# Kernel optimization log

Measured on AMD Instinct MI355X. Metric: run time of the kernel, lower is better.

The kernel has to match this reference:

```python
import jax, jax.numpy as jnp
import numpy as np

NB, S, D, B, T, KMAX = 7, 16, 128, 32, 2048, 31
KS = [31, 21, 15, 11, 7, 5, 3]  # per-band conv kernel sizes


def _ln(x, g, b, eps=1e-5):
    m = x.mean(-1, keepdims=True)
    v = ((x - m) ** 2).mean(-1, keepdims=True)
    return (x - m) * jax.lax.rsqrt(v + eps) * g + b


def setup_inputs() -> dict:
    key = jax.random.key(0)
    ks = jax.random.split(key, 18)
    n = lambda k, shape, s=0.02: jax.random.normal(k, shape, jnp.float32) * s
    # conv kernels zero-padded to KMAX=31; symmetric padding keeps SAME-conv
    # equivalent to Conv1d(kernel=k, padding=k//2)
    mask = np.zeros((NB, KMAX, 1, 1), np.float32)
    for i, k in enumerate(KS):
        off = (KMAX - k) // 2
        mask[i, off:off + k] = 1.0
    inp = {
        'x': jax.random.normal(ks[0], (B, T, S), jnp.float32),
        'conv_w': n(ks[1], (NB, KMAX, S, D)) * jnp.asarray(mask),
        'conv_b': n(ks[2], (NB, D)),
        'dec_g': jnp.ones((NB, D), jnp.float32),
        'dec_b': jnp.zeros((NB, D), jnp.float32),
        'n2_g': jnp.ones((NB, D), jnp.float32),
        'n2_b': jnp.zeros((NB, D), jnp.float32),
        'ffn_w1': n(ks[3], (NB, D, 2 * D)),
        'ffn_b1': n(ks[4], (NB, 2 * D)),
        'ffn_w2': n(ks[5], (NB, 2 * D, D)),
        'ffn_b2': n(ks[6], (NB, D)),
        'proj_w': n(ks[7], (NB, D, 4 * S)),
        'proj_b': n(ks[8], (NB, 4 * S)),
        'mix_w1': n(ks[9], (NB * 4 * S, 8 * S)),
        'mix_b1': n(ks[10], (8 * S,)),
        'mix_w2': n(ks[11], (8 * S, S)),
        'mix_b2': n(ks[12], (S,)),
    }
    return inp


def reference(x, conv_w, conv_b, dec_g, dec_b, n2_g, n2_b,
              ffn_w1, ffn_b1, ffn_w2, ffn_b2,
              proj_w, proj_b, mix_w1, mix_b1, mix_w2, mix_b2):
    # Spectral decomposition: per-band 1D conv + LayerNorm. [nb, B, T, D]
    conv1 = lambda w: jax.lax.conv_general_dilated(
        x, w, (1,), 'SAME', dimension_numbers=('NWC', 'WIO', 'NWC'))
    h = jax.vmap(conv1)(conv_w) + conv_b[:, None, None, :]
    h = _ln(h, dec_g[:, None, None, :], dec_b[:, None, None, :])
    # Band processors (empty history => residual FFN branch)
    z = _ln(h, n2_g[:, None, None, :], n2_b[:, None, None, :])
    u = jax.nn.gelu(jnp.einsum('nbtd,nde->nbte', z, ffn_w1)
                    + ffn_b1[:, None, None, :], approximate=False)
    band_out = h + (jnp.einsum('nbte,ned->nbtd', u, ffn_w2)
                    + ffn_b2[:, None, None, :])
    # Reconstruction: per-band projection, concat, mix MLP
    p = jnp.einsum('nbtd,ndp->nbtp', band_out, proj_w) + proj_b[:, None, None, :]
    cat = jnp.transpose(p, (1, 2, 0, 3)).reshape(x.shape[0], x.shape[1], -1)
    m = jax.nn.gelu(cat @ mix_w1 + mix_b1, approximate=False)
    return m @ mix_w2 + mix_b2
```

## Files before the change

kernel.cpp:

```cpp
#include <hip/hip_runtime.h>
#include <stdint.h>

#define NB   7
#define SIN  16
#define DD   128
#define BB   32
#define TT   2048
#define TM   64
#define KMAX 31

#define XWS  40
#define HS   136
#define US   264
#define PS   72

#define O_CWT 0
#define O_W1T 458752
#define O_W2T 688128
#define O_PT  917504
#define O_M1T 974848
#define O_M2T 1032192
#define W_TOTAL 1034240

typedef short v8s __attribute__((ext_vector_type(8)));
typedef float v4f __attribute__((ext_vector_type(4)));

__device__ __forceinline__ unsigned short f2b(float f) {
    unsigned u = __float_as_uint(f);
    u += 0x7fffu + ((u >> 16) & 1u);
    return (unsigned short)(u >> 16);
}
__device__ __forceinline__ float b2f(unsigned short h) {
    return __uint_as_float(((unsigned)h) << 16);
}
__device__ __forceinline__ float gelu_fast(float x) {
    return x / (1.f + __expf(-1.702f * x));
}
__device__ __forceinline__ float gelu_exact(float x) {
    return 0.5f * x * (1.f + erff(x * 0.70710678118654752f));
}

__global__ void prep_weights(const float* __restrict__ conv_w,
                             const float* __restrict__ ffn_w1,
                             const float* __restrict__ ffn_w2,
                             const float* __restrict__ proj_w,
                             const float* __restrict__ mix_w1,
                             const float* __restrict__ mix_w2,
                             unsigned short* __restrict__ wsb) {
    for (int i = blockIdx.x * 256 + threadIdx.x; i < W_TOTAL; i += gridDim.x * 256) {
        float v;
        int o = i;
        if (o < O_W1T) {
            int n = o / (128 * 512); int r = o % (128 * 512);
            int d = r / 512; int kf = r % 512;
            int k = kf >> 4, s = kf & 15;
            v = (k < KMAX) ? conv_w[((n * KMAX + k) * SIN + s) * DD + d] : 0.f;
        } else if ((o -= O_W1T) < (O_W2T - O_W1T)) {
            int n = o / (256 * 128); int r = o % (256 * 128);
            int e = r / 128; int k = r % 128;
            v = ffn_w1[(n * 128 + k) * 256 + e];
        } else if ((o -= (O_W2T - O_W1T)) < (O_PT - O_W2T)) {
            int n = o / (128 * 256); int r = o % (128 * 256);
            int d = r / 256; int e = r % 256;
            v = ffn_w2[(n * 256 + e) * 128 + d];
        } else if ((o -= (O_PT - O_W2T)) < (O_M1T - O_PT)) {
            int n = o / (64 * 128); int r = o % (64 * 128);
            int j = r / 128; int k = r % 128;
            v = proj_w[(n * 128 + k) * 64 + j];
        } else if ((o -= (O_M1T - O_PT)) < (O_M2T - O_M1T)) {
            int c = o / 448; int kk = o % 448;
            v = mix_w1[kk * 128 + c];
        } else {
            o -= (O_M2T - O_M1T);
            int o16 = o / 128; int c = o % 128;
            v = mix_w2[c * 16 + o16];
        }
        wsb[i] = f2b(v);
    }
}

__global__ __launch_bounds__(256, 2)
void fused_main(const float* __restrict__ x,
                const float* __restrict__ conv_b,
                const float* __restrict__ dec_g, const float* __restrict__ dec_b,
                const float* __restrict__ n2_g,  const float* __restrict__ n2_b,
                const float* __restrict__ ffn_b1, const float* __restrict__ ffn_b2,
                const float* __restrict__ proj_b,
                const float* __restrict__ mix_b1, const float* __restrict__ mix_b2,
                const unsigned short* __restrict__ wsb,
                float* __restrict__ out) {
    __shared__ __align__(16) unsigned short xw[95 * XWS];
    __shared__ __align__(16) unsigned short hbuf[TM * HS];
    __shared__ __align__(16) unsigned short zbuf[TM * HS];
    __shared__ __align__(16) unsigned short ubuf[TM * US];

    const int tid  = threadIdx.x;
    const int lane = tid & 63;
    const int w    = tid >> 6;
    const int l16  = lane & 15;
    const int quad = lane >> 4;
    const int bb   = blockIdx.x >> 5;
    const int t0   = (blockIdx.x & 31) * TM;

    const unsigned short* cwT = wsb + O_CWT;
    const unsigned short* w1T = wsb + O_W1T;
    const unsigned short* w2T = wsb + O_W2T;
    const unsigned short* pT  = wsb + O_PT;
    const unsigned short* m1T = wsb + O_M1T;
    const unsigned short* m2T = wsb + O_M2T;

    for (int i = tid; i < 95 * SIN; i += 256) {
        int r = i >> 4, s = i & 15;
        int t = t0 + r - 15;
        float v = (t >= 0 && t < TT) ? x[((long)bb * TT + t) * SIN + s] : 0.f;
        xw[r * XWS + s] = f2b(v);
    }

    v4f macc[4][2];
    #pragma unroll
    for (int a = 0; a < 4; a++)
        #pragma unroll
        for (int c = 0; c < 2; c++)
            macc[a][c] = (v4f){0.f, 0.f, 0.f, 0.f};

    __syncthreads();

    static const int lo_tab[NB] = {0, 64, 128, 160, 192, 192, 224};
    static const int hi_tab[NB] = {512, 416, 384, 352, 320, 288, 288};

    for (int n = 0; n < NB; ++n) {
        {
            v4f acc[4][2];
            #pragma unroll
            for (int mt = 0; mt < 4; mt++)
                #pragma unroll
                for (int nt = 0; nt < 2; nt++) acc[mt][nt] = (v4f){0.f, 0.f, 0.f, 0.f};
            const int colb = w * 32;
            const int lo = lo_tab[n], hi = hi_tab[n];
            for (int kf = lo; kf < hi; kf += 32) {
                const int tap  = (kf >> 4) + (quad >> 1);
                const int scol = (quad & 1) * 8;
                v8s a[4], bf[2];
                #pragma unroll
                for (int mt = 0; mt < 4; mt++)
                    a[mt] = *reinterpret_cast<const v8s*>(&xw[(mt * 16 + l16 + tap) * XWS + scol]);
                #pragma unroll
                for (int nt = 0; nt < 2; nt++)
                    bf[nt] = *reinterpret_cast<const v8s*>(
                        &cwT[(size_t)(n * 128 + colb + nt * 16 + l16) * 512 + kf + quad * 8]);
                #pragma unroll
                for (int mt = 0; mt < 4; mt++)
                    #pragma unroll
                    for (int nt = 0; nt < 2; nt++)
                        acc[mt][nt] = __builtin_amdgcn_mfma_f32_16x16x32_bf16(a[mt], bf[nt], acc[mt][nt], 0, 0, 0);
            }
            #pragma unroll
            for (int nt = 0; nt < 2; nt++) {
                const int col = colb + nt * 16 + l16;
                const float bias = conv_b[n * 128 + col];
                #pragma unroll
                for (int mt = 0; mt < 4; mt++)
                    #pragma unroll
                    for (int r = 0; r < 4; r++)
                        hbuf[(mt * 16 + quad * 4 + r) * HS + col] = f2b(acc[mt][nt][r] + bias);
            }
        }
        __syncthreads();

        {
            const int row = tid >> 2, q = tid & 3;
            float v[32], s1 = 0.f, s2 = 0.f;
            #pragma unroll
            for (int c8 = 0; c8 < 4; c8++) {
                v8s t8 = *reinterpret_cast<const v8s*>(&hbuf[row * HS + q * 32 + c8 * 8]);
                #pragma unroll
                for (int j = 0; j < 8; j++) {
                    float f = b2f((unsigned short)t8[j]);
                    v[c8 * 8 + j] = f; s1 += f; s2 += f * f;
                }
            }
            s1 += __shfl_xor(s1, 1); s2 += __shfl_xor(s2, 1);
            s1 += __shfl_xor(s1, 2); s2 += __shfl_xor(s2, 2);
            const float m1 = s1 * (1.f / 128.f);
            const float rs = rsqrtf(s2 * (1.f / 128.f) - m1 * m1 + 1e-5f);
            const float4* dg4 = (const float4*)(dec_g + n * 128);
            const float4* db4 = (const float4*)(dec_b + n * 128);
            float hv[32], t1 = 0.f, t2 = 0.f;
            #pragma unroll
            for (int c4 = 0; c4 < 8; c4++) {
                float4 g4 = dg4[q * 8 + c4], b4 = db4[q * 8 + c4];
                float ga[4] = {g4.x, g4.y, g4.z, g4.w};
                float ba[4] = {b4.x, b4.y, b4.z, b4.w};
                #pragma unroll
                for (int j = 0; j < 4; j++) {
                    float h = (v[c4 * 4 + j] - m1) * rs * ga[j] + ba[j];
                    hv[c4 * 4 + j] = h; t1 += h; t2 += h * h;
                    hbuf[row * HS + q * 32 + c4 * 4 + j] = f2b(h);
                }
            }
            t1 += __shfl_xor(t1, 1); t2 += __shfl_xor(t2, 1);
            t1 += __shfl_xor(t1, 2); t2 += __shfl_xor(t2, 2);
            const float m2 = t1 * (1.f / 128.f);
            const float rs2 = rsqrtf(t2 * (1.f / 128.f) - m2 * m2 + 1e-5f);
            const float4* ng4 = (const float4*)(n2_g + n * 128);
            const float4* nb4 = (const float4*)(n2_b + n * 128);
            #pragma unroll
            for (int c4 = 0; c4 < 8; c4++) {
                float4 g4 = ng4[q * 8 + c4], b4 = nb4[q * 8 + c4];
                float ga[4] = {g4.x, g4.y, g4.z, g4.w};
                float ba[4] = {b4.x, b4.y, b4.z, b4.w};
                #pragma unroll
                for (int j = 0; j < 4; j++) {
                    float z = (hv[c4 * 4 + j] - m2) * rs2 * ga[j] + ba[j];
                    zbuf[row * HS + q * 32 + c4 * 4 + j] = f2b(z);
                }
            }
        }
        __syncthreads();

        {
            v4f acc[4][4];
            #pragma unroll
            for (int mt = 0; mt < 4; mt++)
                #pragma unroll
                for (int et = 0; et < 4; et++) acc[mt][et] = (v4f){0.f, 0.f, 0.f, 0.f};
            const int eb = w * 64;
            #pragma unroll
            for (int kb = 0; kb < 128; kb += 32) {
                v8s a[4], bf[4];
                #pragma unroll
                for (int mt = 0; mt < 4; mt++)
                    a[mt] = *reinterpret_cast<const v8s*>(&zbuf[(mt * 16 + l16) * HS + kb + quad * 8]);
                #pragma unroll
                for (int et = 0; et < 4; et++)
                    bf[et] = *reinterpret_cast<const v8s*>(
                        &w1T[(size_t)(n * 256 + eb + et * 16 + l16) * 128 + kb + quad * 8]);
                #pragma unroll
                for (int mt = 0; mt < 4; mt++)
                    #pragma unroll
                    for (int et = 0; et < 4; et++)
                        acc[mt][et] = __builtin_amdgcn_mfma_f32_16x16x32_bf16(a[mt], bf[et], acc[mt][et], 0, 0, 0);
            }
            #pragma unroll
            for (int et = 0; et < 4; et++) {
                const int e = eb + et * 16 + l16;
                const float bias = ffn_b1[n * 256 + e];
                #pragma unroll
                for (int mt = 0; mt < 4; mt++)
                    #pragma unroll
                    for (int r = 0; r < 4; r++)
                        ubuf[(mt * 16 + quad * 4 + r) * US + e] = f2b(gelu_fast(acc[mt][et][r] + bias));
            }
        }
        __syncthreads();

        {
            v4f acc[4][2];
            #pragma unroll
            for (int mt = 0; mt < 4; mt++)
                #pragma unroll
                for (int nt = 0; nt < 2; nt++) acc[mt][nt] = (v4f){0.f, 0.f, 0.f, 0.f};
            const int dbs = w * 32;
            #pragma unroll
            for (int kb = 0; kb < 256; kb += 32) {
                v8s a[4], bf[2];
                #pragma unroll
                for (int mt = 0; mt < 4; mt++)
                    a[mt] = *reinterpret_cast<const v8s*>(&ubuf[(mt * 16 + l16) * US + kb + quad * 8]);
                #pragma unroll
                for (int nt = 0; nt < 2; nt++)
                    bf[nt] = *reinterpret_cast<const v8s*>(
                        &w2T[(size_t)(n * 128 + dbs + nt * 16 + l16) * 256 + kb + quad * 8]);
                #pragma unroll
                for (int mt = 0; mt < 4; mt++)
                    #pragma unroll
                    for (int nt = 0; nt < 2; nt++)
                        acc[mt][nt] = __builtin_amdgcn_mfma_f32_16x16x32_bf16(a[mt], bf[nt], acc[mt][nt], 0, 0, 0);
            }
            #pragma unroll
            for (int nt = 0; nt < 2; nt++) {
                const int col = dbs + nt * 16 + l16;
                const float bias = ffn_b2[n * 128 + col];
                #pragma unroll
                for (int mt = 0; mt < 4; mt++)
                    #pragma unroll
                    for (int r = 0; r < 4; r++) {
                        const int row = mt * 16 + quad * 4 + r;
                        float bo = acc[mt][nt][r] + bias + b2f(hbuf[row * HS + col]);
                        zbuf[row * HS + col] = f2b(bo);
                    }
            }
        }
        __syncthreads();

        {
            v4f acc[4];
            #pragma unroll
            for (int mt = 0; mt < 4; mt++) acc[mt] = (v4f){0.f, 0.f, 0.f, 0.f};
            const int j = w * 16 + l16;
            #pragma unroll
            for (int kb = 0; kb < 128; kb += 32) {
                v8s bf = *reinterpret_cast<const v8s*>(&pT[(size_t)(n * 64 + j) * 128 + kb + quad * 8]);
                #pragma unroll
                for (int mt = 0; mt < 4; mt++) {
                    v8s a = *reinterpret_cast<const v8s*>(&zbuf[(mt * 16 + l16) * HS + kb + quad * 8]);
                    acc[mt] = __builtin_amdgcn_mfma_f32_16x16x32_bf16(a, bf, acc[mt], 0, 0, 0);
                }
            }
            const float bias = proj_b[n * 64 + j];
            unsigned short* pb = ubuf;
            #pragma unroll
            for (int mt = 0; mt < 4; mt++)
                #pragma unroll
                for (int r = 0; r < 4; r++)
                    pb[(mt * 16 + quad * 4 + r) * PS + j] = f2b(acc[mt][r] + bias);
        }
        __syncthreads();

        {
            const unsigned short* pb = ubuf;
            #pragma unroll
            for (int kb = 0; kb < 64; kb += 32) {
                v8s a[4], bf[2];
                #pragma unroll
                for (int mt = 0; mt < 4; mt++)
                    a[mt] = *reinterpret_cast<const v8s*>(&pb[(mt * 16 + l16) * PS + kb + quad * 8]);
                #pragma unroll
                for (int nt = 0; nt < 2; nt++)
                    bf[nt] = *reinterpret_cast<const v8s*>(
                        &m1T[(size_t)(w * 32 + nt * 16 + l16) * 448 + n * 64 + kb + quad * 8]);
                #pragma unroll
                for (int mt = 0; mt < 4; mt++)
                    #pragma unroll
                    for (int nt = 0; nt < 2; nt++)
                        macc[mt][nt] = __builtin_amdgcn_mfma_f32_16x16x32_bf16(a[mt], bf[nt], macc[mt][nt], 0, 0, 0);
            }
        }
    }

    #pragma unroll
    for (int nt = 0; nt < 2; nt++) {
        const int col = w * 32 + nt * 16 + l16;
        const float bias = mix_b1[col];
        #pragma unroll
        for (int mt = 0; mt < 4; mt++)
            #pragma unroll
            for (int r = 0; r < 4; r++)
                zbuf[(mt * 16 + quad * 4 + r) * HS + col] = f2b(gelu_exact(macc[mt][nt][r] + bias));
    }
    __syncthreads();

    {
        v4f acc = (v4f){0.f, 0.f, 0.f, 0.f};
        #pragma unroll
        for (int kb = 0; kb < 128; kb += 32) {
            v8s a  = *reinterpret_cast<const v8s*>(&zbuf[(w * 16 + l16) * HS + kb + quad * 8]);
            v8s bf = *reinterpret_cast<const v8s*>(&m2T[(size_t)l16 * 128 + kb + quad * 8]);
            acc = __builtin_amdgcn_mfma_f32_16x16x32_bf16(a, bf, acc, 0, 0, 0);
        }
        const float bias = mix_b2[l16];
        #pragma unroll
        for (int r = 0; r < 4; r++) {
            const int row = w * 16 + quad * 4 + r;
            out[((long)bb * TT + t0 + row) * SIN + l16] = acc[r] + bias;
        }
    }
}

extern "C" void kernel_launch(void* const* d_in, const int* in_sizes, int n_in,
                              void* d_out, int out_size, void* d_ws, size_t ws_size,
                              hipStream_t stream) {
    (void)in_sizes; (void)n_in; (void)out_size; (void)ws_size;
    const float* x      = (const float*)d_in[0];
    const float* conv_w = (const float*)d_in[1];
    const float* conv_b = (const float*)d_in[2];
    const float* dec_g  = (const float*)d_in[3];
    const float* dec_b  = (const float*)d_in[4];
    const float* n2_g   = (const float*)d_in[5];
    const float* n2_b   = (const float*)d_in[6];
    const float* ffn_w1 = (const float*)d_in[7];
    const float* ffn_b1 = (const float*)d_in[8];
    const float* ffn_w2 = (const float*)d_in[9];
    const float* ffn_b2 = (const float*)d_in[10];
    const float* proj_w = (const float*)d_in[11];
    const float* proj_b = (const float*)d_in[12];
    const float* mix_w1 = (const float*)d_in[13];
    const float* mix_b1 = (const float*)d_in[14];
    const float* mix_w2 = (const float*)d_in[15];
    const float* mix_b2 = (const float*)d_in[16];
    unsigned short* wsb = (unsigned short*)d_ws;
    float* out = (float*)d_out;

    hipLaunchKernelGGL(prep_weights, dim3(512), dim3(256), 0, stream,
                       conv_w, ffn_w1, ffn_w2, proj_w, mix_w1, mix_w2, wsb);
    hipLaunchKernelGGL(fused_main, dim3(BB * (TT / TM)), dim3(256), 0, stream,
                       x, conv_b, dec_g, dec_b, n2_g, n2_b, ffn_b1, ffn_b2,
                       proj_b, mix_b1, mix_b2, wsb, out);
}
```

Baseline: 418.4 us.

## Split work across 8 waves with 2x4 row/column wave tiling per block

Doubles the block to 512 threads and splits each GEMM stage's 64-row tile across two wave rows, so each wave computes 32 rows instead of 64. The LayerNorm stage now uses 8 threads per row with an extra shuffle step. This halves per-wave accumulator registers and raises the number of resident waves to hide latency. In exchange, each weight (B-operand) fragment is loaded by twice as many waves, so global/L2 weight traffic per block doubles, and block-wide barriers now synchronise more waves.

```diff
diff --git a/kernel.cpp b/kernel.cpp
--- a/kernel.cpp
+++ b/kernel.cpp
@@ -79,7 +79,7 @@
     }
 }
 
-__global__ __launch_bounds__(256, 2)
+__global__ __launch_bounds__(512, 4)
 void fused_main(const float* __restrict__ x,
                 const float* __restrict__ conv_b,
                 const float* __restrict__ dec_g, const float* __restrict__ dec_b,
@@ -97,6 +97,8 @@
     const int tid  = threadIdx.x;
     const int lane = tid & 63;
     const int w    = tid >> 6;
+    const int wm   = w >> 2;
+    const int wn   = w & 3;
     const int l16  = lane & 15;
     const int quad = lane >> 4;
     const int bb   = blockIdx.x >> 5;
@@ -109,16 +111,18 @@
     const unsigned short* m1T = wsb + O_M1T;
     const unsigned short* m2T = wsb + O_M2T;
 
-    for (int i = tid; i < 95 * SIN; i += 256) {
+    const int rowb = wm * 32;
+
+    for (int i = tid; i < 95 * SIN; i += 512) {
         int r = i >> 4, s = i & 15;
         int t = t0 + r - 15;
         float v = (t >= 0 && t < TT) ? x[((long)bb * TT + t) * SIN + s] : 0.f;
         xw[r * XWS + s] = f2b(v);
     }
 
-    v4f macc[4][2];
+    v4f macc[2][2];
     #pragma unroll
-    for (int a = 0; a < 4; a++)
+    for (int a = 0; a < 2; a++)
         #pragma unroll
         for (int c = 0; c < 2; c++)
             macc[a][c] = (v4f){0.f, 0.f, 0.f, 0.f};
@@ -130,26 +134,26 @@
 
     for (int n = 0; n < NB; ++n) {
         {
-            v4f acc[4][2];
-            #pragma unroll
-            for (int mt = 0; mt < 4; mt++)
+            v4f acc[2][2];
+            #pragma unroll
+            for (int mt = 0; mt < 2; mt++)
                 #pragma unroll
                 for (int nt = 0; nt < 2; nt++) acc[mt][nt] = (v4f){0.f, 0.f, 0.f, 0.f};
-            const int colb = w * 32;
+            const int colb = wn * 32;
             const int lo = lo_tab[n], hi = hi_tab[n];
             for (int kf = lo; kf < hi; kf += 32) {
                 const int tap  = (kf >> 4) + (quad >> 1);
                 const int scol = (quad & 1) * 8;
-                v8s a[4], bf[2];
-                #pragma unroll
-                for (int mt = 0; mt < 4; mt++)
-                    a[mt] = *reinterpret_cast<const v8s*>(&xw[(mt * 16 + l16 + tap) * XWS + scol]);
+                v8s a[2], bf[2];
+                #pragma unroll
+                for (int mt = 0; mt < 2; mt++)
+                    a[mt] = *reinterpret_cast<const v8s*>(&xw[(rowb + mt * 16 + l16 + tap) * XWS + scol]);
                 #pragma unroll
                 for (int nt = 0; nt < 2; nt++)
                     bf[nt] = *reinterpret_cast<const v8s*>(
                         &cwT[(size_t)(n * 128 + colb + nt * 16 + l16) * 512 + kf + quad * 8]);
                 #pragma unroll
-                for (int mt = 0; mt < 4; mt++)
+                for (int mt = 0; mt < 2; mt++)
                     #pragma unroll
                     for (int nt = 0; nt < 2; nt++)
                         acc[mt][nt] = __builtin_amdgcn_mfma_f32_16x16x32_bf16(a[mt], bf[nt], acc[mt][nt], 0, 0, 0);
@@ -159,20 +163,20 @@
                 const int col = colb + nt * 16 + l16;
                 const float bias = conv_b[n * 128 + col];
                 #pragma unroll
-                for (int mt = 0; mt < 4; mt++)
+                for (int mt = 0; mt < 2; mt++)
                     #pragma unroll
                     for (int r = 0; r < 4; r++)
-                        hbuf[(mt * 16 + quad * 4 + r) * HS + col] = f2b(acc[mt][nt][r] + bias);
+                        hbuf[(rowb + mt * 16 + quad * 4 + r) * HS + col] = f2b(acc[mt][nt][r] + bias);
             }
         }
         __syncthreads();
 
         {
-            const int row = tid >> 2, q = tid & 3;
-            float v[32], s1 = 0.f, s2 = 0.f;
-            #pragma unroll
-            for (int c8 = 0; c8 < 4; c8++) {
-                v8s t8 = *reinterpret_cast<const v8s*>(&hbuf[row * HS + q * 32 + c8 * 8]);
+            const int row = tid >> 3, q = tid & 7;
+            float v[16], s1 = 0.f, s2 = 0.f;
+            #pragma unroll
+            for (int c8 = 0; c8 < 2; c8++) {
+                v8s t8 = *reinterpret_cast<const v8s*>(&hbuf[row * HS + q * 16 + c8 * 8]);
                 #pragma unroll
                 for (int j = 0; j < 8; j++) {
                     float f = b2f((unsigned short)t8[j]);
@@ -181,62 +185,64 @@
             }
             s1 += __shfl_xor(s1, 1); s2 += __shfl_xor(s2, 1);
             s1 += __shfl_xor(s1, 2); s2 += __shfl_xor(s2, 2);
+            s1 += __shfl_xor(s1, 4); s2 += __shfl_xor(s2, 4);
             const float m1 = s1 * (1.f / 128.f);
             const float rs = rsqrtf(s2 * (1.f / 128.f) - m1 * m1 + 1e-5f);
             const float4* dg4 = (const float4*)(dec_g + n * 128);
             const float4* db4 = (const float4*)(dec_b + n * 128);
-            float hv[32], t1 = 0.f, t2 = 0.f;
-            #pragma unroll
-            for (int c4 = 0; c4 < 8; c4++) {
-                float4 g4 = dg4[q * 8 + c4], b4 = db4[q * 8 + c4];
+            float hv[16], t1 = 0.f, t2 = 0.f;
+            #pragma unroll
+            for (int c4 = 0; c4 < 4; c4++) {
+                float4 g4 = dg4[q * 4 + c4], b4 = db4[q * 4 + c4];
                 float ga[4] = {g4.x, g4.y, g4.z, g4.w};
                 float ba[4] = {b4.x, b4.y, b4.z, b4.w};
                 #pragma unroll
                 for (int j = 0; j < 4; j++) {
                     float h = (v[c4 * 4 + j] - m1) * rs * ga[j] + ba[j];
                     hv[c4 * 4 + j] = h; t1 += h; t2 += h * h;
-                    hbuf[row * HS + q * 32 + c4 * 4 + j] = f2b(h);
+                    hbuf[row * HS + q * 16 + c4 * 4 + j] = f2b(h);
                 }
             }
             t1 += __shfl_xor(t1, 1); t2 += __shfl_xor(t2, 1);
             t1 += __shfl_xor(t1, 2); t2 += __shfl_xor(t2, 2);
+            t1 += __shfl_xor(t1, 4); t2 += __shfl_xor(t2, 4);
             const float m2 = t1 * (1.f / 128.f);
             const float rs2 = rsqrtf(t2 * (1.f / 128.f) - m2 * m2 + 1e-5f);
             const float4* ng4 = (const float4*)(n2_g + n * 128);
             const float4* nb4 = (const float4*)(n2_b + n * 128);
             #pragma unroll
-            for (int c4 = 0; c4 < 8; c4++) {
-                float4 g4 = ng4[q * 8 + c4], b4 = nb4[q * 8 + c4];
+            for (int c4 = 0; c4 < 4; c4++) {
+                float4 g4 = ng4[q * 4 + c4], b4 = nb4[q * 4 + c4];
                 float ga[4] = {g4.x, g4.y, g4.z, g4.w};
                 float ba[4] = {b4.x, b4.y, b4.z, b4.w};
                 #pragma unroll
                 for (int j = 0; j < 4; j++) {
                     float z = (hv[c4 * 4 + j] - m2) * rs2 * ga[j] + ba[j];
-                    zbuf[row * HS + q * 32 + c4 * 4 + j] = f2b(z);
+                    zbuf[row * HS + q * 16 + c4 * 4 + j] = f2b(z);
                 }
             }
         }
         __syncthreads();
 
         {
-            v4f acc[4][4];
-            #pragma unroll
-            for (int mt = 0; mt < 4; mt++)
+            v4f acc[2][4];
+            #pragma unroll
+            for (int mt = 0; mt < 2; mt++)
                 #pragma unroll
                 for (int et = 0; et < 4; et++) acc[mt][et] = (v4f){0.f, 0.f, 0.f, 0.f};
-            const int eb = w * 64;
+            const int eb = wn * 64;
             #pragma unroll
             for (int kb = 0; kb < 128; kb += 32) {
-                v8s a[4], bf[4];
-                #pragma unroll
-                for (int mt = 0; mt < 4; mt++)
-                    a[mt] = *reinterpret_cast<const v8s*>(&zbuf[(mt * 16 + l16) * HS + kb + quad * 8]);
+                v8s a[2], bf[4];
+                #pragma unroll
+                for (int mt = 0; mt < 2; mt++)
+                    a[mt] = *reinterpret_cast<const v8s*>(&zbuf[(rowb + mt * 16 + l16) * HS + kb + quad * 8]);
                 #pragma unroll
                 for (int et = 0; et < 4; et++)
                     bf[et] = *reinterpret_cast<const v8s*>(
                         &w1T[(size_t)(n * 256 + eb + et * 16 + l16) * 128 + kb + quad * 8]);
                 #pragma unroll
-                for (int mt = 0; mt < 4; mt++)
+                for (int mt = 0; mt < 2; mt++)
                     #pragma unroll
                     for (int et = 0; et < 4; et++)
                         acc[mt][et] = __builtin_amdgcn_mfma_f32_16x16x32_bf16(a[mt], bf[et], acc[mt][et], 0, 0, 0);
@@ -246,33 +252,33 @@
                 const int e = eb + et * 16 + l16;
                 const float bias = ffn_b1[n * 256 + e];
                 #pragma unroll
-                for (int mt = 0; mt < 4; mt++)
+                for (int mt = 0; mt < 2; mt++)
                     #pragma unroll
                     for (int r = 0; r < 4; r++)
-                        ubuf[(mt * 16 + quad * 4 + r) * US + e] = f2b(gelu_fast(acc[mt][et][r] + bias));
+                        ubuf[(rowb + mt * 16 + quad * 4 + r) * US + e] = f2b(gelu_fast(acc[mt][et][r] + bias));
             }
         }
         __syncthreads();
 
         {
-            v4f acc[4][2];
-            #pragma unroll
-            for (int mt = 0; mt < 4; mt++)
+            v4f acc[2][2];
+            #pragma unroll
+            for (int mt = 0; mt < 2; mt++)
                 #pragma unroll
                 for (int nt = 0; nt < 2; nt++) acc[mt][nt] = (v4f){0.f, 0.f, 0.f, 0.f};
-            const int dbs = w * 32;
+            const int dbs = wn * 32;
             #pragma unroll
             for (int kb = 0; kb < 256; kb += 32) {
-                v8s a[4], bf[2];
-                #pragma unroll
-                for (int mt = 0; mt < 4; mt++)
-                    a[mt] = *reinterpret_cast<const v8s*>(&ubuf[(mt * 16 + l16) * US + kb + quad * 8]);
+                v8s a[2], bf[2];
+                #pragma unroll
+                for (int mt = 0; mt < 2; mt++)
+                    a[mt] = *reinterpret_cast<const v8s*>(&ubuf[(rowb + mt * 16 + l16) * US + kb + quad * 8]);
                 #pragma unroll
                 for (int nt = 0; nt < 2; nt++)
                     bf[nt] = *reinterpret_cast<const v8s*>(
                         &w2T[(size_t)(n * 128 + dbs + nt * 16 + l16) * 256 + kb + quad * 8]);
                 #pragma unroll
-                for (int mt = 0; mt < 4; mt++)
+                for (int mt = 0; mt < 2; mt++)
                     #pragma unroll
                     for (int nt = 0; nt < 2; nt++)
                         acc[mt][nt] = __builtin_amdgcn_mfma_f32_16x16x32_bf16(a[mt], bf[nt], acc[mt][nt], 0, 0, 0);
@@ -282,10 +288,10 @@
                 const int col = dbs + nt * 16 + l16;
                 const float bias = ffn_b2[n * 128 + col];
                 #pragma unroll
-                for (int mt = 0; mt < 4; mt++)
+                for (int mt = 0; mt < 2; mt++)
                     #pragma unroll
                     for (int r = 0; r < 4; r++) {
-                        const int row = mt * 16 + quad * 4 + r;
+                        const int row = rowb + mt * 16 + quad * 4 + r;
                         float bo = acc[mt][nt][r] + bias + b2f(hbuf[row * HS + col]);
                         zbuf[row * HS + col] = f2b(bo);
                     }
@@ -294,26 +300,26 @@
         __syncthreads();
 
         {
-            v4f acc[4];
-            #pragma unroll
-            for (int mt = 0; mt < 4; mt++) acc[mt] = (v4f){0.f, 0.f, 0.f, 0.f};
-            const int j = w * 16 + l16;
+            v4f acc[2];
+            #pragma unroll
+            for (int mt = 0; mt < 2; mt++) acc[mt] = (v4f){0.f, 0.f, 0.f, 0.f};
+            const int j = wn * 16 + l16;
             #pragma unroll
             for (int kb = 0; kb < 128; kb += 32) {
                 v8s bf = *reinterpret_cast<const v8s*>(&pT[(size_t)(n * 64 + j) * 128 + kb + quad * 8]);
                 #pragma unroll
-                for (int mt = 0; mt < 4; mt++) {
-                    v8s a = *reinterpret_cast<const v8s*>(&zbuf[(mt * 16 + l16) * HS + kb + quad * 8]);
+                for (int mt = 0; mt < 2; mt++) {
+                    v8s a = *reinterpret_cast<const v8s*>(&zbuf[(rowb + mt * 16 + l16) * HS + kb + quad * 8]);
                     acc[mt] = __builtin_amdgcn_mfma_f32_16x16x32_bf16(a, bf, acc[mt], 0, 0, 0);
                 }
             }
             const float bias = proj_b[n * 64 + j];
             unsigned short* pb = ubuf;
             #pragma unroll
-            for (int mt = 0; mt < 4; mt++)
+            for (int mt = 0; mt < 2; mt++)
                 #pragma unroll
                 for (int r = 0; r < 4; r++)
-                    pb[(mt * 16 + quad * 4 + r) * PS + j] = f2b(acc[mt][r] + bias);
+                    pb[(rowb + mt * 16 + quad * 4 + r) * PS + j] = f2b(acc[mt][r] + bias);
         }
         __syncthreads();
 
@@ -321,16 +327,16 @@
             const unsigned short* pb = ubuf;
             #pragma unroll
             for (int kb = 0; kb < 64; kb += 32) {
-                v8s a[4], bf[2];
-                #pragma unroll
-                for (int mt = 0; mt < 4; mt++)
-                    a[mt] = *reinterpret_cast<const v8s*>(&pb[(mt * 16 + l16) * PS + kb + quad * 8]);
+                v8s a[2], bf[2];
+                #pragma unroll
+                for (int mt = 0; mt < 2; mt++)
+                    a[mt] = *reinterpret_cast<const v8s*>(&pb[(rowb + mt * 16 + l16) * PS + kb + quad * 8]);
                 #pragma unroll
                 for (int nt = 0; nt < 2; nt++)
                     bf[nt] = *reinterpret_cast<const v8s*>(
-                        &m1T[(size_t)(w * 32 + nt * 16 + l16) * 448 + n * 64 + kb + quad * 8]);
-                #pragma unroll
-                for (int mt = 0; mt < 4; mt++)
+                        &m1T[(size_t)(wn * 32 + nt * 16 + l16) * 448 + n * 64 + kb + quad * 8]);
+                #pragma unroll
+                for (int mt = 0; mt < 2; mt++)
                     #pragma unroll
                     for (int nt = 0; nt < 2; nt++)
                         macc[mt][nt] = __builtin_amdgcn_mfma_f32_16x16x32_bf16(a[mt], bf[nt], macc[mt][nt], 0, 0, 0);
@@ -340,17 +346,17 @@
 
     #pragma unroll
     for (int nt = 0; nt < 2; nt++) {
-        const int col = w * 32 + nt * 16 + l16;
+        const int col = wn * 32 + nt * 16 + l16;
         const float bias = mix_b1[col];
         #pragma unroll
-        for (int mt = 0; mt < 4; mt++)
+        for (int mt = 0; mt < 2; mt++)
             #pragma unroll
             for (int r = 0; r < 4; r++)
-                zbuf[(mt * 16 + quad * 4 + r) * HS + col] = f2b(gelu_exact(macc[mt][nt][r] + bias));
+                zbuf[(rowb + mt * 16 + quad * 4 + r) * HS + col] = f2b(gelu_exact(macc[mt][nt][r] + bias));
     }
     __syncthreads();
 
-    {
+    if (w < 4) {
         v4f acc = (v4f){0.f, 0.f, 0.f, 0.f};
         #pragma unroll
         for (int kb = 0; kb < 128; kb += 32) {
@@ -393,7 +399,7 @@
 
     hipLaunchKernelGGL(prep_weights, dim3(512), dim3(256), 0, stream,
                        conv_w, ffn_w1, ffn_w2, proj_w, mix_w1, mix_w2, wsb);
-    hipLaunchKernelGGL(fused_main, dim3(BB * (TT / TM)), dim3(256), 0, stream,
+    hipLaunchKernelGGL(fused_main, dim3(BB * (TT / TM)), dim3(512), 0, stream,
                        x, conv_b, dec_g, dec_b, n2_g, n2_b, ffn_b1, ffn_b2,
                        proj_b, mix_b1, mix_b2, wsb, out);
 }
```

New measurement: 536.2 us. +28.2%, slower.

## Fold per-band projection into mix_w1 to skip projection GEMM

Applied to the files above, without the earlier changes.

Precomputes combined weights Wc[n] = proj_w[n] @ mix_w1[n-slice] and a combined bias (mix_b1 + proj_b @ mix_w1) in the weight-prep kernel. The fused kernel then feeds band_out straight into the mix accumulation, with K=128 per band. This removes the projection MFMA stage, its LDS round trip and one barrier per band. In exchange, per-band mix MFMAs double (K 64→128), the fused bias is stored as bf16, and prep does a small extra matmul.

```diff
diff --git a/kernel.cpp b/kernel.cpp
--- a/kernel.cpp
+++ b/kernel.cpp
@@ -12,15 +12,14 @@
 #define XWS  40
 #define HS   136
 #define US   264
-#define PS   72
 
 #define O_CWT 0
 #define O_W1T 458752
 #define O_W2T 688128
-#define O_PT  917504
-#define O_M1T 974848
+#define O_WCT 917504
 #define O_M2T 1032192
-#define W_TOTAL 1034240
+#define O_B1A 1034240
+#define W_TOTAL 1034368
 
 typedef short v8s __attribute__((ext_vector_type(8)));
 typedef float v4f __attribute__((ext_vector_type(4)));
@@ -46,6 +45,8 @@
                              const float* __restrict__ proj_w,
                              const float* __restrict__ mix_w1,
                              const float* __restrict__ mix_w2,
+                             const float* __restrict__ proj_b,
+                             const float* __restrict__ mix_b1,
                              unsigned short* __restrict__ wsb) {
     for (int i = blockIdx.x * 256 + threadIdx.x; i < W_TOTAL; i += gridDim.x * 256) {
         float v;
@@ -59,21 +60,34 @@
             int n = o / (256 * 128); int r = o % (256 * 128);
             int e = r / 128; int k = r % 128;
             v = ffn_w1[(n * 128 + k) * 256 + e];
-        } else if ((o -= (O_W2T - O_W1T)) < (O_PT - O_W2T)) {
+        } else if ((o -= (O_W2T - O_W1T)) < (O_WCT - O_W2T)) {
             int n = o / (128 * 256); int r = o % (128 * 256);
             int d = r / 256; int e = r % 256;
             v = ffn_w2[(n * 256 + e) * 128 + d];
-        } else if ((o -= (O_PT - O_W2T)) < (O_M1T - O_PT)) {
-            int n = o / (64 * 128); int r = o % (64 * 128);
-            int j = r / 128; int k = r % 128;
-            v = proj_w[(n * 128 + k) * 64 + j];
-        } else if ((o -= (O_M1T - O_PT)) < (O_M2T - O_M1T)) {
-            int c = o / 448; int kk = o % 448;
-            v = mix_w1[kk * 128 + c];
-        } else {
-            o -= (O_M2T - O_M1T);
+        } else if ((o -= (O_WCT - O_W2T)) < (O_M2T - O_WCT)) {
+            int n = o / (128 * 128); int r = o % (128 * 128);
+            int c = r / 128; int k = r % 128;
+            const float4* pw4 = (const float4*)(proj_w + ((size_t)(n * 128 + k)) * 64);
+            float s = 0.f;
+            #pragma unroll 4
+            for (int j4 = 0; j4 < 16; j4++) {
+                float4 p4 = pw4[j4];
+                int jb = n * 64 + j4 * 4;
+                s += p4.x * mix_w1[(jb + 0) * 128 + c]
+                   + p4.y * mix_w1[(jb + 1) * 128 + c]
+                   + p4.z * mix_w1[(jb + 2) * 128 + c]
+                   + p4.w * mix_w1[(jb + 3) * 128 + c];
+            }
+            v = s;
+        } else if ((o -= (O_M2T - O_WCT)) < (O_B1A - O_M2T)) {
             int o16 = o / 128; int c = o % 128;
             v = mix_w2[c * 16 + o16];
+        } else {
+            o -= (O_B1A - O_M2T);
+            float s = mix_b1[o];
+            for (int kk = 0; kk < 448; kk++)
+                s += proj_b[kk] * mix_w1[kk * 128 + o];
+            v = s;
         }
         wsb[i] = f2b(v);
     }
@@ -85,10 +99,9 @@
                 const float* __restrict__ dec_g, const float* __restrict__ dec_b,
                 const float* __restrict__ n2_g,  const float* __restrict__ n2_b,
                 const float* __restrict__ ffn_b1, const float* __restrict__ ffn_b2,
-                const float* __restrict__ proj_b,
-                const float* __restrict__ mix_b1, const float* __restrict__ mix_b2,
                 const unsigned short* __restrict__ wsb,
-                float* __restrict__ out) {
+                float* __restrict__ out,
+                const float* __restrict__ mix_b2) {
     __shared__ __align__(16) unsigned short xw[95 * XWS];
     __shared__ __align__(16) unsigned short hbuf[TM * HS];
     __shared__ __align__(16) unsigned short zbuf[TM * HS];
@@ -105,8 +118,7 @@
     const unsigned short* cwT = wsb + O_CWT;
     const unsigned short* w1T = wsb + O_W1T;
     const unsigned short* w2T = wsb + O_W2T;
-    const unsigned short* pT  = wsb + O_PT;
-    const unsigned short* m1T = wsb + O_M1T;
+    const unsigned short* wcT = wsb + O_WCT;
     const unsigned short* m2T = wsb + O_M2T;
 
     for (int i = tid; i < 95 * SIN; i += 256) {
@@ -294,41 +306,16 @@
         __syncthreads();
 
         {
-            v4f acc[4];
-            #pragma unroll
-            for (int mt = 0; mt < 4; mt++) acc[mt] = (v4f){0.f, 0.f, 0.f, 0.f};
-            const int j = w * 16 + l16;
             #pragma unroll
             for (int kb = 0; kb < 128; kb += 32) {
-                v8s bf = *reinterpret_cast<const v8s*>(&pT[(size_t)(n * 64 + j) * 128 + kb + quad * 8]);
-                #pragma unroll
-                for (int mt = 0; mt < 4; mt++) {
-                    v8s a = *reinterpret_cast<const v8s*>(&zbuf[(mt * 16 + l16) * HS + kb + quad * 8]);
-                    acc[mt] = __builtin_amdgcn_mfma_f32_16x16x32_bf16(a, bf, acc[mt], 0, 0, 0);
-                }
-            }
-            const float bias = proj_b[n * 64 + j];
-            unsigned short* pb = ubuf;
-            #pragma unroll
-            for (int mt = 0; mt < 4; mt++)
-                #pragma unroll
-                for (int r = 0; r < 4; r++)
-                    pb[(mt * 16 + quad * 4 + r) * PS + j] = f2b(acc[mt][r] + bias);
-        }
-        __syncthreads();
-
-        {
-            const unsigned short* pb = ubuf;
-            #pragma unroll
-            for (int kb = 0; kb < 64; kb += 32) {
                 v8s a[4], bf[2];
                 #pragma unroll
                 for (int mt = 0; mt < 4; mt++)
-                    a[mt] = *reinterpret_cast<const v8s*>(&pb[(mt * 16 + l16) * PS + kb + quad * 8]);
+                    a[mt] = *reinterpret_cast<const v8s*>(&zbuf[(mt * 16 + l16) * HS + kb + quad * 8]);
                 #pragma unroll
                 for (int nt = 0; nt < 2; nt++)
                     bf[nt] = *reinterpret_cast<const v8s*>(
-                        &m1T[(size_t)(w * 32 + nt * 16 + l16) * 448 + n * 64 + kb + quad * 8]);
+                        &wcT[(size_t)(n * 128 + w * 32 + nt * 16 + l16) * 128 + kb + quad * 8]);
                 #pragma unroll
                 for (int mt = 0; mt < 4; mt++)
                     #pragma unroll
@@ -341,7 +328,7 @@
     #pragma unroll
     for (int nt = 0; nt < 2; nt++) {
         const int col = w * 32 + nt * 16 + l16;
-        const float bias = mix_b1[col];
+        const float bias = b2f(wsb[O_B1A + col]);
         #pragma unroll
         for (int mt = 0; mt < 4; mt++)
             #pragma unroll
@@ -392,8 +379,9 @@
     float* out = (float*)d_out;
 
     hipLaunchKernelGGL(prep_weights, dim3(512), dim3(256), 0, stream,
-                       conv_w, ffn_w1, ffn_w2, proj_w, mix_w1, mix_w2, wsb);
+                       conv_w, ffn_w1, ffn_w2, proj_w, mix_w1, mix_w2,
+                       proj_b, mix_b1, wsb);
     hipLaunchKernelGGL(fused_main, dim3(BB * (TT / TM)), dim3(256), 0, stream,
                        x, conv_b, dec_g, dec_b, n2_g, n2_b, ffn_b1, ffn_b2,
-                       proj_b, mix_b1, mix_b2, wsb, out);
-}
+                       wsb, out, mix_b2);
+}
```

New measurement: 426.5 us. Within noise of the previous version (+1.9%).
